# Kernel tuning notes

Measured on AMD Instinct MI355X. Metric: run time of the kernel, lower is better.

Reference implementation:

```python
import jax, jax.numpy as jnp
import numpy as np
import math

B = 2
H = 16
M = 1024
D = 64      # head_dim
P = 1024    # persistent memory size
SPAN = 1024 # external attention span


def setup_inputs() -> dict:
    key = jax.random.key(0)
    k1, k2, k3, k4 = jax.random.split(key, 4)
    query = jax.random.normal(k1, (B * H, M, D), dtype=jnp.float32)
    attn = jax.random.normal(k2, (B * H, M, SPAN), dtype=jnp.float32)
    # params as in __init__
    pkey = jax.random.normal(k3, (H, D, P), dtype=jnp.float32) / math.sqrt(D)
    pval = jax.random.normal(k4, (H, P, D), dtype=jnp.float32) / math.sqrt(P)
    return {"query": query, "attn": attn, "key": pkey, "val": pval}


def reference(query, attn, key, val):
    h, d, p = key.shape
    bh, m, _ = query.shape
    q = query.reshape(-1, h, m, d)                      # [B,H,M,D]
    # attn_pers = q @ (key * sqrt(d)); later divided by sqrt(d) -> net q@key
    attn_pers = jnp.einsum('bhmd,hdp->bhmp', q, key * math.sqrt(d))
    attn_pers = attn_pers.reshape(-1, m, p)             # [B*H,M,P]
    scores = jnp.concatenate([attn, attn_pers], axis=-1) / math.sqrt(d)
    probs = jax.nn.softmax(scores, axis=-1)             # [B*H,M,SPAN+P]
    attn_out = probs[:, :, :-p]                         # [B*H,M,SPAN]
    pers = probs[:, :, -p:].reshape(-1, h, m, p)        # [B,H,M,P]
    out = jnp.einsum('bhmp,hpd->bhmd', pers, val * math.sqrt(p))
    out = out.reshape(-1, m, d)                         # [B*H,M,D]
    return (attn_out, out)
```

## Files before the change

### kernel.cpp

```cpp
#include <hip/hip_runtime.h>
#include <hip/hip_bf16.h>
#include <math.h>

#define BH   32
#define NH   16
#define MM   1024
#define DD   64
#define PP   1024
#define SPAN 1024

typedef unsigned short ushort_t;
typedef __attribute__((ext_vector_type(8))) short  short8;
typedef __attribute__((ext_vector_type(4))) float  f32x4;

#define MFMA(a,b,c) __builtin_amdgcn_mfma_f32_16x16x32_bf16(a,b,c,0,0,0)

#if __has_builtin(__builtin_amdgcn_exp2f)
#define EXP2(x) __builtin_amdgcn_exp2f(x)
#else
#define EXP2(x) __expf((x) * 0.6931471805599453f)
#endif

#define ATTN_SC 0.18033688011111603f
#define LOG2E   1.4426950408889634f

#define WS_SA_OFF  (4194304ull)
#define WS_SP0_OFF (4325376ull)
#define WS_SP1_OFF (4456448ull)
#define WS_O1_OFF  (4587520ull)
#define WS_NEED    (12976128ull)

__device__ __forceinline__ ushort_t f2bf(float x) {
    __hip_bfloat16 b = __float2bfloat16(x);
    return __builtin_bit_cast(unsigned short, b);
}
__device__ __forceinline__ float bf2f(ushort_t u) {
    __hip_bfloat16 b = __builtin_bit_cast(__hip_bfloat16, u);
    return __bfloat162float(b);
}

__launch_bounds__(256)
__global__ void pm_pre(const float* __restrict__ key,
                       const float* __restrict__ val,
                       ushort_t* __restrict__ wsKV)
{
    int bi = blockIdx.x, t = threadIdx.x;
    if (bi < 512) {
        int id = bi * 256 + t;
        int l  = id & 63;
        int ks = (id >> 6) & 1;
        int pb = (id >> 7) & 3;
        int c  = (id >> 9) & 15;
        int h  = (id >> 13) & 15;
        int p     = c * 64 + pb * 16 + (l & 15);
        int dbase = ks * 32 + (l >> 4) * 8;
        size_t fo = (size_t)(h * 16 + c) * 8192 + (size_t)(pb * 2 + ks) * 512 + (size_t)l * 8;
#pragma unroll
        for (int e = 0; e < 8; ++e)
            wsKV[fo + e] = f2bf(key[(size_t)(h * 64 + dbase + e) * PP + p] * LOG2E);
    } else {
        int id = (bi - 512) * 256 + t;
        int l   = id & 63;
        int db  = (id >> 6) & 3;
        int ks2 = (id >> 8) & 1;
        int c   = (id >> 9) & 15;
        int h   = (id >> 13) & 15;
        int d = db * 16 + (l & 15);
        size_t fo = (size_t)(h * 16 + c) * 8192 + 4096 + (size_t)(ks2 * 4 + db) * 512 + (size_t)l * 8;
#pragma unroll
        for (int e = 0; e < 8; ++e) {
            int p = c * 64 + ks2 * 32 + ((l >> 4) * 4) + (e & 3) + 16 * (e >> 2);
            wsKV[fo + e] = f2bf(val[(size_t)(h * PP + p) * DD + d]);
        }
    }
}

__launch_bounds__(256)
__global__ void pm_work(const float* __restrict__ q,
                        const float* __restrict__ attn,
                        const ushort_t* __restrict__ wsKV,
                        float* __restrict__ ws_sa,
                        float* __restrict__ ws_sp0,
                        float* __restrict__ ws_sp1,
                        float* __restrict__ o1,
                        float* __restrict__ out)
{
    __shared__ ushort_t kvbuf[2][8192];

    const int t  = threadIdx.x;
    const int w  = t >> 6;
    const int l  = t & 63;
    const int bi = blockIdx.x;
    const int hi = l >> 4;
    const int lo = l & 15;

    const int ty   = bi % 3;
    const int unit = bi / 3;
    const int bh   = unit & 31;
    const int tile = unit >> 5;
    const size_t rowbase = (size_t)bh * MM + tile * 64;

    if (ty < 2) {
        const int s = ty;
        const int h = bh & (NH - 1);

        short8 qf[2][2];
        {
            const float* qr = q + (rowbase + w * 16 + lo) * DD + hi * 8;
#pragma unroll
            for (int ks = 0; ks < 2; ++ks) {
                float4 a = *(const float4*)(qr + ks * 32);
                float4 b = *(const float4*)(qr + ks * 32 + 4);
                float f[8] = {a.x, a.y, a.z, a.w, b.x, b.y, b.z, b.w};
                short8 qh, ql;
#pragma unroll
                for (int e = 0; e < 8; ++e) {
                    ushort_t hh = f2bf(f[e]);
                    qh[e] = (short)hh;
                    ql[e] = (short)f2bf(f[e] - bf2f(hh));
                }
                qf[ks][0] = qh;
                qf[ks][1] = ql;
            }
        }

        const ushort_t* KVb = wsKV + (size_t)h * (16 * 8192);

        auto STAGE = [&](int b, int c) {
            const char* src = (const char*)(KVb + (size_t)c * 8192) + w * 4096 + l * 16;
            char* dst = (char*)&kvbuf[b][0] + w * 4096;
#pragma unroll
            for (int j = 0; j < 4; ++j)
                __builtin_amdgcn_global_load_lds(
                    (const __attribute__((address_space(1))) void*)(src + j * 1024),
                    (__attribute__((address_space(3))) void*)(dst + j * 1024),
                    16, 0, 0);
        };

        f32x4 oacc[4] = {{0.f,0.f,0.f,0.f},{0.f,0.f,0.f,0.f},{0.f,0.f,0.f,0.f},{0.f,0.f,0.f,0.f}};
        float spart = 0.f;

        STAGE(0, s * 8);
        __syncthreads();

        for (int cc = 0; cc < 8; ++cc) {
            const int cur = cc & 1;
            if (cc < 7) STAGE(cur ^ 1, s * 8 + cc + 1);

            const ushort_t* Kc = &kvbuf[cur][0];
            const ushort_t* Vc = Kc + 4096;

            f32x4 sacc[4] = {{0.f,0.f,0.f,0.f},{0.f,0.f,0.f,0.f},{0.f,0.f,0.f,0.f},{0.f,0.f,0.f,0.f}};
            __builtin_amdgcn_s_setprio(1);
#pragma unroll
            for (int pb = 0; pb < 4; ++pb) {
#pragma unroll
                for (int ks = 0; ks < 2; ++ks) {
                    short8 khi = *(const short8*)(Kc + (pb * 2 + ks) * 512 + l * 8);
                    sacc[pb] = MFMA(khi, qf[ks][0], sacc[pb]);
                    sacc[pb] = MFMA(khi, qf[ks][1], sacc[pb]);
                }
            }
            __builtin_amdgcn_s_setprio(0);

            float ep[4][4];
#pragma unroll
            for (int pb = 0; pb < 4; ++pb)
#pragma unroll
                for (int r = 0; r < 4; ++r) {
                    float pv = EXP2(sacc[pb][r]);
                    ep[pb][r] = pv;
                    spart += pv;
                }

            short8 pf[2][2];
#pragma unroll
            for (int ks2 = 0; ks2 < 2; ++ks2) {
                short8 phi8, plo8;
#pragma unroll
                for (int e = 0; e < 8; ++e) {
                    float pv = ep[ks2 * 2 + (e >> 2)][e & 3];
                    ushort_t hh = f2bf(pv);
                    phi8[e] = (short)hh;
                    plo8[e] = (short)f2bf(pv - bf2f(hh));
                }
                pf[ks2][0] = phi8;
                pf[ks2][1] = plo8;
            }

            __builtin_amdgcn_s_setprio(1);
#pragma unroll
            for (int ks2 = 0; ks2 < 2; ++ks2) {
#pragma unroll
                for (int db = 0; db < 4; ++db) {
                    short8 vhi = *(const short8*)(Vc + (ks2 * 4 + db) * 512 + l * 8);
                    oacc[db] = MFMA(pf[ks2][0], vhi, oacc[db]);
                    oacc[db] = MFMA(pf[ks2][1], vhi, oacc[db]);
                }
            }
            __builtin_amdgcn_s_setprio(0);

            __syncthreads();
        }

        spart += __shfl_xor(spart, 16);
        spart += __shfl_xor(spart, 32);
        float* spdst = s ? ws_sp1 : ws_sp0;
        if (hi == 0) spdst[rowbase + w * 16 + lo] = spart;

        float* odst = s ? o1 : out;
#pragma unroll
        for (int reg = 0; reg < 4; ++reg) {
            const size_t ro = (rowbase + w * 16 + hi * 4 + reg) * DD + lo;
#pragma unroll
            for (int db = 0; db < 4; ++db)
                __builtin_nontemporal_store(oacc[db][reg], &odst[ro + db * 16]);
        }
    } else {
        for (int rp = 0; rp < 8; ++rp) {
            const int r0 = w * 16 + rp * 2;
            const f32x4* a0 = (const f32x4*)(attn + (rowbase + r0) * SPAN);
            const f32x4* a1 = (const f32x4*)(attn + (rowbase + r0 + 1) * SPAN);
            f32x4 v0[4], v1[4];
#pragma unroll
            for (int j = 0; j < 4; ++j) v0[j] = a0[j * 64 + l];
#pragma unroll
            for (int j = 0; j < 4; ++j) v1[j] = a1[j * 64 + l];

            float s0 = 0.f, s1 = 0.f;
#pragma unroll
            for (int j = 0; j < 4; ++j)
#pragma unroll
                for (int e = 0; e < 4; ++e) {
                    s0 += EXP2(v0[j][e] * ATTN_SC);
                    s1 += EXP2(v1[j][e] * ATTN_SC);
                }
#pragma unroll
            for (int s = 1; s < 64; s <<= 1) {
                s0 += __shfl_xor(s0, s);
                s1 += __shfl_xor(s1, s);
            }
            if (l == 0) {
                ws_sa[rowbase + r0]     = s0;
                ws_sa[rowbase + r0 + 1] = s1;
            }
        }
    }
}

__launch_bounds__(256)
__global__ void pm_norm(const float* __restrict__ attn,
                        const float* __restrict__ ws_sa,
                        const float* __restrict__ ws_sp0,
                        const float* __restrict__ ws_sp1,
                        const float* __restrict__ o1,
                        float* __restrict__ attn_out,
                        float* __restrict__ out)
{
    const int t = threadIdx.x;
    const int w = t >> 6;
    const int l = t & 63;
    const size_t row = (size_t)blockIdx.x * 4 + w;

    const float iZ = 1.f / (ws_sa[row] + ws_sp0[row] + ws_sp1[row]);

    const f32x4* arow = (const f32x4*)(attn + row * SPAN);
    f32x4 av[4];
#pragma unroll
    for (int j = 0; j < 4; ++j) av[j] = arow[j * 64 + l];
    const float ov0 = out[row * DD + l];
    const float ov1 = o1[row * DD + l];

    f32x4* orow = (f32x4*)(attn_out + row * SPAN);
#pragma unroll
    for (int j = 0; j < 4; ++j) {
        f32x4 o;
#pragma unroll
        for (int e = 0; e < 4; ++e) o[e] = EXP2(av[j][e] * ATTN_SC) * iZ;
        __builtin_nontemporal_store(o, orow + j * 64 + l);
    }
    __builtin_nontemporal_store((ov0 + ov1) * 32.f * iZ, &out[row * DD + l]);
}

__launch_bounds__(256)
__global__ void pm_fallback(const float* __restrict__ q,
                            const float* __restrict__ attn,
                            const float* __restrict__ key,
                            const float* __restrict__ val,
                            float* __restrict__ attn_out,
                            float* __restrict__ out)
{
    __shared__ float qs[64][68];
    __shared__ float ks[64][68];
    __shared__ float vs[64][DD];
    __shared__ float sc[64][66];
    __shared__ float rmax[64];
    __shared__ float rsum[64];

    const int t    = threadIdx.x;
    const int bh   = blockIdx.y;
    const int tile = blockIdx.x;
    const int h    = bh & (NH - 1);
    const int m0   = tile * 64;
    const int tr   = t >> 4;
    const int tc   = t & 15;
    const int r0   = tr * 4;
    const int c0   = tc * 4;
    const int lane = t & 63;
    const int wave = t >> 6;

    const size_t qbase = (size_t)bh * MM * DD + (size_t)m0 * DD;
    const size_t abase = (size_t)bh * MM * SPAN + (size_t)m0 * SPAN;
    const size_t kbase = (size_t)h * DD * PP;
    const size_t vbase = (size_t)h * PP * DD;

#pragma unroll
    for (int j = 0; j < 16; ++j) {
        int idx = j * 256 + t;
        int r = idx >> 6, d = idx & 63;
        qs[r][d] = q[qbase + (size_t)r * DD + d];
    }
    for (int rr = 0; rr < 16; ++rr) {
        int r = wave * 16 + rr;
        const float* arow = attn + abase + (size_t)r * SPAN;
        float av[16];
        float mx = -INFINITY;
#pragma unroll
        for (int j = 0; j < 16; ++j) { av[j] = arow[j * 64 + lane] * 0.125f; mx = fmaxf(mx, av[j]); }
#pragma unroll
        for (int s = 32; s; s >>= 1) mx = fmaxf(mx, __shfl_xor(mx, s));
        float sm = 0.f;
#pragma unroll
        for (int j = 0; j < 16; ++j) sm += __expf(av[j] - mx);
#pragma unroll
        for (int s = 32; s; s >>= 1) sm += __shfl_xor(sm, s);
        if (lane == 0) { rmax[r] = mx; rsum[r] = sm; }
    }
    __syncthreads();
    for (int p0 = 0; p0 < PP; p0 += 64) {
        if (p0) __syncthreads();
#pragma unroll
        for (int j = 0; j < 16; ++j) {
            int idx = j * 256 + t;
            int d = idx >> 6, pc = idx & 63;
            ks[pc][d] = key[kbase + (size_t)d * PP + p0 + pc];
        }
        __syncthreads();
        float acc[4][4] = {};
#pragma unroll
        for (int d0 = 0; d0 < DD; d0 += 4) {
            float4 q4[4], k4[4];
#pragma unroll
            for (int rr = 0; rr < 4; ++rr) q4[rr] = *(const float4*)&qs[r0 + rr][d0];
#pragma unroll
            for (int cc = 0; cc < 4; ++cc) k4[cc] = *(const float4*)&ks[c0 + cc][d0];
#pragma unroll
            for (int rr = 0; rr < 4; ++rr)
#pragma unroll
                for (int cc = 0; cc < 4; ++cc)
                    acc[rr][cc] += q4[rr].x * k4[cc].x + q4[rr].y * k4[cc].y
                                 + q4[rr].z * k4[cc].z + q4[rr].w * k4[cc].w;
        }
#pragma unroll
        for (int rr = 0; rr < 4; ++rr) {
            float mx = fmaxf(fmaxf(acc[rr][0], acc[rr][1]), fmaxf(acc[rr][2], acc[rr][3]));
#pragma unroll
            for (int s = 8; s; s >>= 1) mx = fmaxf(mx, __shfl_xor(mx, s));
            float sm = 0.f;
#pragma unroll
            for (int cc = 0; cc < 4; ++cc) sm += __expf(acc[rr][cc] - mx);
#pragma unroll
            for (int s = 8; s; s >>= 1) sm += __shfl_xor(sm, s);
            if (tc == 0) {
                int r = r0 + rr;
                float om = rmax[r], os = rsum[r];
                float nm = fmaxf(om, mx);
                rsum[r] = os * __expf(om - nm) + sm * __expf(mx - nm);
                rmax[r] = nm;
            }
        }
    }
    __syncthreads();
    for (int rr = 0; rr < 16; ++rr) {
        int r = wave * 16 + rr;
        float Mx = rmax[r];
        float iZ = 1.0f / rsum[r];
        const float* arow = attn + abase + (size_t)r * SPAN;
        float* orow = attn_out + abase + (size_t)r * SPAN;
#pragma unroll
        for (int j = 0; j < 16; ++j) {
            float a = arow[j * 64 + lane] * 0.125f;
            orow[j * 64 + lane] = __expf(a - Mx) * iZ;
        }
    }
    float acc2[4][4] = {};
    for (int p0 = 0; p0 < PP; p0 += 64) {
        __syncthreads();
#pragma unroll
        for (int j = 0; j < 16; ++j) {
            int idx = j * 256 + t;
            int d = idx >> 6, pc = idx & 63;
            ks[pc][d] = key[kbase + (size_t)d * PP + p0 + pc];
        }
#pragma unroll
        for (int j = 0; j < 16; ++j) {
            int idx = j * 256 + t;
            int pc = idx >> 6, d = idx & 63;
            vs[pc][d] = val[vbase + (size_t)(p0 + pc) * DD + d];
        }
        __syncthreads();
        float acc[4][4] = {};
#pragma unroll
        for (int d0 = 0; d0 < DD; d0 += 4) {
            float4 q4[4], k4[4];
#pragma unroll
            for (int rr = 0; rr < 4; ++rr) q4[rr] = *(const float4*)&qs[r0 + rr][d0];
#pragma unroll
            for (int cc = 0; cc < 4; ++cc) k4[cc] = *(const float4*)&ks[c0 + cc][d0];
#pragma unroll
            for (int rr = 0; rr < 4; ++rr)
#pragma unroll
                for (int cc = 0; cc < 4; ++cc)
                    acc[rr][cc] += q4[rr].x * k4[cc].x + q4[rr].y * k4[cc].y
                                 + q4[rr].z * k4[cc].z + q4[rr].w * k4[cc].w;
        }
#pragma unroll
        for (int rr = 0; rr < 4; ++rr) {
            float Mx = rmax[r0 + rr];
#pragma unroll
            for (int cc = 0; cc < 4; ++cc)
                sc[r0 + rr][c0 + cc] = __expf(acc[rr][cc] - Mx);
        }
        __syncthreads();
        for (int pc = 0; pc < 64; ++pc) {
            float4 v4 = *(const float4*)&vs[pc][tc * 4];
#pragma unroll
            for (int rr = 0; rr < 4; ++rr) {
                float pr = sc[r0 + rr][pc];
                acc2[rr][0] += pr * v4.x;
                acc2[rr][1] += pr * v4.y;
                acc2[rr][2] += pr * v4.z;
                acc2[rr][3] += pr * v4.w;
            }
        }
    }
#pragma unroll
    for (int rr = 0; rr < 4; ++rr) {
        int r = r0 + rr;
        float s = 32.0f / rsum[r];
        float4 o;
        o.x = acc2[rr][0] * s; o.y = acc2[rr][1] * s;
        o.z = acc2[rr][2] * s; o.w = acc2[rr][3] * s;
        *(float4*)&out[(size_t)bh * MM * DD + (size_t)(m0 + r) * DD + tc * 4] = o;
    }
}

extern "C" void kernel_launch(void* const* d_in, const int* in_sizes, int n_in,
                              void* d_out, int out_size, void* d_ws, size_t ws_size,
                              hipStream_t stream) {
    const float* q    = (const float*)d_in[0];
    const float* attn = (const float*)d_in[1];
    const float* key  = (const float*)d_in[2];
    const float* val  = (const float*)d_in[3];
    float* attn_out = (float*)d_out;
    float* out      = (float*)d_out + (size_t)BH * MM * SPAN;

    if (ws_size >= WS_NEED) {
        ushort_t* wsKV   = (ushort_t*)d_ws;
        float*    ws_sa  = (float*)((char*)d_ws + WS_SA_OFF);
        float*    ws_sp0 = (float*)((char*)d_ws + WS_SP0_OFF);
        float*    ws_sp1 = (float*)((char*)d_ws + WS_SP1_OFF);
        float*    o1     = (float*)((char*)d_ws + WS_O1_OFF);
        pm_pre <<<1024, 256, 0, stream>>>(key, val, wsKV);
        pm_work<<<1536, 256, 0, stream>>>(q, attn, wsKV, ws_sa, ws_sp0, ws_sp1, o1, out);
        pm_norm<<<8192, 256, 0, stream>>>(attn, ws_sa, ws_sp0, ws_sp1, o1, attn_out, out);
    } else {
        dim3 grid(MM / 64, BH);
        pm_fallback<<<grid, 256, 0, stream>>>(q, attn, key, val, attn_out, out);
    }
}
```

Before: 87.85 us.

## Fuse attn row-sum into normalization kernel to avoid re-reading attn

```diff
diff --git a/kernel.cpp b/kernel.cpp
--- a/kernel.cpp
+++ b/kernel.cpp
@@ -24,11 +24,10 @@
 #define ATTN_SC 0.18033688011111603f
 #define LOG2E   1.4426950408889634f
 
-#define WS_SA_OFF  (4194304ull)
-#define WS_SP0_OFF (4325376ull)
-#define WS_SP1_OFF (4456448ull)
-#define WS_O1_OFF  (4587520ull)
-#define WS_NEED    (12976128ull)
+#define WS_SP0_OFF (4194304ull)
+#define WS_SP1_OFF (4325376ull)
+#define WS_O1_OFF  (4456448ull)
+#define WS_NEED    (12845056ull)
 
 __device__ __forceinline__ ushort_t f2bf(float x) {
     __hip_bfloat16 b = __float2bfloat16(x);
@@ -76,14 +75,12 @@
 }
 
 __launch_bounds__(256)
-__global__ void pm_work(const float* __restrict__ q,
-                        const float* __restrict__ attn,
-                        const ushort_t* __restrict__ wsKV,
-                        float* __restrict__ ws_sa,
-                        float* __restrict__ ws_sp0,
-                        float* __restrict__ ws_sp1,
-                        float* __restrict__ o1,
-                        float* __restrict__ out)
+__global__ void pm_flash(const float* __restrict__ q,
+                         const ushort_t* __restrict__ wsKV,
+                         float* __restrict__ ws_sp0,
+                         float* __restrict__ ws_sp1,
+                         float* __restrict__ o1,
+                         float* __restrict__ out)
 {
     __shared__ ushort_t kvbuf[2][8192];
 
@@ -94,163 +91,129 @@
     const int hi = l >> 4;
     const int lo = l & 15;
 
-    const int ty   = bi % 3;
-    const int unit = bi / 3;
+    const int s    = bi & 1;
+    const int unit = bi >> 1;
     const int bh   = unit & 31;
     const int tile = unit >> 5;
+    const int h    = bh & (NH - 1);
     const size_t rowbase = (size_t)bh * MM + tile * 64;
 
-    if (ty < 2) {
-        const int s = ty;
-        const int h = bh & (NH - 1);
-
-        short8 qf[2][2];
-        {
-            const float* qr = q + (rowbase + w * 16 + lo) * DD + hi * 8;
+    short8 qf[2][2];
+    {
+        const float* qr = q + (rowbase + w * 16 + lo) * DD + hi * 8;
+#pragma unroll
+        for (int ks = 0; ks < 2; ++ks) {
+            float4 a = *(const float4*)(qr + ks * 32);
+            float4 b = *(const float4*)(qr + ks * 32 + 4);
+            float f[8] = {a.x, a.y, a.z, a.w, b.x, b.y, b.z, b.w};
+            short8 qh, ql;
+#pragma unroll
+            for (int e = 0; e < 8; ++e) {
+                ushort_t hh = f2bf(f[e]);
+                qh[e] = (short)hh;
+                ql[e] = (short)f2bf(f[e] - bf2f(hh));
+            }
+            qf[ks][0] = qh;
+            qf[ks][1] = ql;
+        }
+    }
+
+    const ushort_t* KVb = wsKV + (size_t)h * (16 * 8192);
+
+    auto STAGE = [&](int b, int c) {
+        const char* src = (const char*)(KVb + (size_t)c * 8192) + w * 4096 + l * 16;
+        char* dst = (char*)&kvbuf[b][0] + w * 4096;
+#pragma unroll
+        for (int j = 0; j < 4; ++j)
+            __builtin_amdgcn_global_load_lds(
+                (const __attribute__((address_space(1))) void*)(src + j * 1024),
+                (__attribute__((address_space(3))) void*)(dst + j * 1024),
+                16, 0, 0);
+    };
+
+    f32x4 oacc[4] = {{0.f,0.f,0.f,0.f},{0.f,0.f,0.f,0.f},{0.f,0.f,0.f,0.f},{0.f,0.f,0.f,0.f}};
+    float spart = 0.f;
+
+    STAGE(0, s * 8);
+    __syncthreads();
+
+    for (int cc = 0; cc < 8; ++cc) {
+        const int cur = cc & 1;
+        if (cc < 7) STAGE(cur ^ 1, s * 8 + cc + 1);
+
+        const ushort_t* Kc = &kvbuf[cur][0];
+        const ushort_t* Vc = Kc + 4096;
+
+        f32x4 sacc[4] = {{0.f,0.f,0.f,0.f},{0.f,0.f,0.f,0.f},{0.f,0.f,0.f,0.f},{0.f,0.f,0.f,0.f}};
+        __builtin_amdgcn_s_setprio(1);
+#pragma unroll
+        for (int pb = 0; pb < 4; ++pb) {
 #pragma unroll
             for (int ks = 0; ks < 2; ++ks) {
-                float4 a = *(const float4*)(qr + ks * 32);
-                float4 b = *(const float4*)(qr + ks * 32 + 4);
-                float f[8] = {a.x, a.y, a.z, a.w, b.x, b.y, b.z, b.w};
-                short8 qh, ql;
-#pragma unroll
-                for (int e = 0; e < 8; ++e) {
-                    ushort_t hh = f2bf(f[e]);
-                    qh[e] = (short)hh;
-                    ql[e] = (short)f2bf(f[e] - bf2f(hh));
-                }
-                qf[ks][0] = qh;
-                qf[ks][1] = ql;
-            }
-        }
-
-        const ushort_t* KVb = wsKV + (size_t)h * (16 * 8192);
-
-        auto STAGE = [&](int b, int c) {
-            const char* src = (const char*)(KVb + (size_t)c * 8192) + w * 4096 + l * 16;
-            char* dst = (char*)&kvbuf[b][0] + w * 4096;
-#pragma unroll
-            for (int j = 0; j < 4; ++j)
-                __builtin_amdgcn_global_load_lds(
-                    (const __attribute__((address_space(1))) void*)(src + j * 1024),
-                    (__attribute__((address_space(3))) void*)(dst + j * 1024),
-                    16, 0, 0);
-        };
-
-        f32x4 oacc[4] = {{0.f,0.f,0.f,0.f},{0.f,0.f,0.f,0.f},{0.f,0.f,0.f,0.f},{0.f,0.f,0.f,0.f}};
-        float spart = 0.f;
-
-        STAGE(0, s * 8);
+                short8 khi = *(const short8*)(Kc + (pb * 2 + ks) * 512 + l * 8);
+                sacc[pb] = MFMA(khi, qf[ks][0], sacc[pb]);
+                sacc[pb] = MFMA(khi, qf[ks][1], sacc[pb]);
+            }
+        }
+        __builtin_amdgcn_s_setprio(0);
+
+        float ep[4][4];
+#pragma unroll
+        for (int pb = 0; pb < 4; ++pb)
+#pragma unroll
+            for (int r = 0; r < 4; ++r) {
+                float pv = EXP2(sacc[pb][r]);
+                ep[pb][r] = pv;
+                spart += pv;
+            }
+
+        short8 pf[2][2];
+#pragma unroll
+        for (int ks2 = 0; ks2 < 2; ++ks2) {
+            short8 phi8, plo8;
+#pragma unroll
+            for (int e = 0; e < 8; ++e) {
+                float pv = ep[ks2 * 2 + (e >> 2)][e & 3];
+                ushort_t hh = f2bf(pv);
+                phi8[e] = (short)hh;
+                plo8[e] = (short)f2bf(pv - bf2f(hh));
+            }
+            pf[ks2][0] = phi8;
+            pf[ks2][1] = plo8;
+        }
+
+        __builtin_amdgcn_s_setprio(1);
+#pragma unroll
+        for (int ks2 = 0; ks2 < 2; ++ks2) {
+#pragma unroll
+            for (int db = 0; db < 4; ++db) {
+                short8 vhi = *(const short8*)(Vc + (ks2 * 4 + db) * 512 + l * 8);
+                oacc[db] = MFMA(pf[ks2][0], vhi, oacc[db]);
+                oacc[db] = MFMA(pf[ks2][1], vhi, oacc[db]);
+            }
+        }
+        __builtin_amdgcn_s_setprio(0);
+
         __syncthreads();
-
-        for (int cc = 0; cc < 8; ++cc) {
-            const int cur = cc & 1;
-            if (cc < 7) STAGE(cur ^ 1, s * 8 + cc + 1);
-
-            const ushort_t* Kc = &kvbuf[cur][0];
-            const ushort_t* Vc = Kc + 4096;
-
-            f32x4 sacc[4] = {{0.f,0.f,0.f,0.f},{0.f,0.f,0.f,0.f},{0.f,0.f,0.f,0.f},{0.f,0.f,0.f,0.f}};
-            __builtin_amdgcn_s_setprio(1);
-#pragma unroll
-            for (int pb = 0; pb < 4; ++pb) {
-#pragma unroll
-                for (int ks = 0; ks < 2; ++ks) {
-                    short8 khi = *(const short8*)(Kc + (pb * 2 + ks) * 512 + l * 8);
-                    sacc[pb] = MFMA(khi, qf[ks][0], sacc[pb]);
-                    sacc[pb] = MFMA(khi, qf[ks][1], sacc[pb]);
-                }
-            }
-            __builtin_amdgcn_s_setprio(0);
-
-            float ep[4][4];
-#pragma unroll
-            for (int pb = 0; pb < 4; ++pb)
-#pragma unroll
-                for (int r = 0; r < 4; ++r) {
-                    float pv = EXP2(sacc[pb][r]);
-                    ep[pb][r] = pv;
-                    spart += pv;
-                }
-
-            short8 pf[2][2];
-#pragma unroll
-            for (int ks2 = 0; ks2 < 2; ++ks2) {
-                short8 phi8, plo8;
-#pragma unroll
-                for (int e = 0; e < 8; ++e) {
-                    float pv = ep[ks2 * 2 + (e >> 2)][e & 3];
-                    ushort_t hh = f2bf(pv);
-                    phi8[e] = (short)hh;
-                    plo8[e] = (short)f2bf(pv - bf2f(hh));
-                }
-                pf[ks2][0] = phi8;
-                pf[ks2][1] = plo8;
-            }
-
-            __builtin_amdgcn_s_setprio(1);
-#pragma unroll
-            for (int ks2 = 0; ks2 < 2; ++ks2) {
-#pragma unroll
-                for (int db = 0; db < 4; ++db) {
-                    short8 vhi = *(const short8*)(Vc + (ks2 * 4 + db) * 512 + l * 8);
-                    oacc[db] = MFMA(pf[ks2][0], vhi, oacc[db]);
-                    oacc[db] = MFMA(pf[ks2][1], vhi, oacc[db]);
-                }
-            }
-            __builtin_amdgcn_s_setprio(0);
-
-            __syncthreads();
-        }
-
-        spart += __shfl_xor(spart, 16);
-        spart += __shfl_xor(spart, 32);
-        float* spdst = s ? ws_sp1 : ws_sp0;
-        if (hi == 0) spdst[rowbase + w * 16 + lo] = spart;
-
-        float* odst = s ? o1 : out;
-#pragma unroll
-        for (int reg = 0; reg < 4; ++reg) {
-            const size_t ro = (rowbase + w * 16 + hi * 4 + reg) * DD + lo;
-#pragma unroll
-            for (int db = 0; db < 4; ++db)
-                __builtin_nontemporal_store(oacc[db][reg], &odst[ro + db * 16]);
-        }
-    } else {
-        for (int rp = 0; rp < 8; ++rp) {
-            const int r0 = w * 16 + rp * 2;
-            const f32x4* a0 = (const f32x4*)(attn + (rowbase + r0) * SPAN);
-            const f32x4* a1 = (const f32x4*)(attn + (rowbase + r0 + 1) * SPAN);
-            f32x4 v0[4], v1[4];
-#pragma unroll
-            for (int j = 0; j < 4; ++j) v0[j] = a0[j * 64 + l];
-#pragma unroll
-            for (int j = 0; j < 4; ++j) v1[j] = a1[j * 64 + l];
-
-            float s0 = 0.f, s1 = 0.f;
-#pragma unroll
-            for (int j = 0; j < 4; ++j)
-#pragma unroll
-                for (int e = 0; e < 4; ++e) {
-                    s0 += EXP2(v0[j][e] * ATTN_SC);
-                    s1 += EXP2(v1[j][e] * ATTN_SC);
-                }
-#pragma unroll
-            for (int s = 1; s < 64; s <<= 1) {
-                s0 += __shfl_xor(s0, s);
-                s1 += __shfl_xor(s1, s);
-            }
-            if (l == 0) {
-                ws_sa[rowbase + r0]     = s0;
-                ws_sa[rowbase + r0 + 1] = s1;
-            }
-        }
+    }
+
+    spart += __shfl_xor(spart, 16);
+    spart += __shfl_xor(spart, 32);
+    float* spdst = s ? ws_sp1 : ws_sp0;
+    if (hi == 0) spdst[rowbase + w * 16 + lo] = spart;
+
+    float* odst = s ? o1 : out;
+#pragma unroll
+    for (int reg = 0; reg < 4; ++reg) {
+        const size_t ro = (rowbase + w * 16 + hi * 4 + reg) * DD + lo;
+#pragma unroll
+        for (int db = 0; db < 4; ++db)
+            __builtin_nontemporal_store(oacc[db][reg], &odst[ro + db * 16]);
     }
 }
 
 __launch_bounds__(256)
 __global__ void pm_norm(const float* __restrict__ attn,
-                        const float* __restrict__ ws_sa,
                         const float* __restrict__ ws_sp0,
                         const float* __restrict__ ws_sp1,
                         const float* __restrict__ o1,
@@ -262,23 +225,31 @@
     const int l = t & 63;
     const size_t row = (size_t)blockIdx.x * 4 + w;
 
-    const float iZ = 1.f / (ws_sa[row] + ws_sp0[row] + ws_sp1[row]);
-
     const f32x4* arow = (const f32x4*)(attn + row * SPAN);
     f32x4 av[4];
 #pragma unroll
     for (int j = 0; j < 4; ++j) av[j] = arow[j * 64 + l];
+
+    float sm = 0.f;
+#pragma unroll
+    for (int j = 0; j < 4; ++j)
+#pragma unroll
+        for (int e = 0; e < 4; ++e) {
+            av[j][e] = EXP2(av[j][e] * ATTN_SC);
+            sm += av[j][e];
+        }
+#pragma unroll
+    for (int s = 1; s < 64; s <<= 1) sm += __shfl_xor(sm, s);
+
+    const float iZ = 1.f / (sm + ws_sp0[row] + ws_sp1[row]);
+
+    f32x4* orow = (f32x4*)(attn_out + row * SPAN);
+#pragma unroll
+    for (int j = 0; j < 4; ++j)
+        __builtin_nontemporal_store(av[j] * iZ, orow + j * 64 + l);
+
     const float ov0 = out[row * DD + l];
     const float ov1 = o1[row * DD + l];
-
-    f32x4* orow = (f32x4*)(attn_out + row * SPAN);
-#pragma unroll
-    for (int j = 0; j < 4; ++j) {
-        f32x4 o;
-#pragma unroll
-        for (int e = 0; e < 4; ++e) o[e] = EXP2(av[j][e] * ATTN_SC) * iZ;
-        __builtin_nontemporal_store(o, orow + j * 64 + l);
-    }
     __builtin_nontemporal_store((ov0 + ov1) * 32.f * iZ, &out[row * DD + l]);
 }
 
@@ -384,13 +355,13 @@
     for (int rr = 0; rr < 16; ++rr) {
         int r = wave * 16 + rr;
         float Mx = rmax[r];
-        float iZ = 1.0f / rsum[r];
+        float iZv = 1.0f / rsum[r];
         const float* arow = attn + abase + (size_t)r * SPAN;
         float* orow = attn_out + abase + (size_t)r * SPAN;
 #pragma unroll
         for (int j = 0; j < 16; ++j) {
             float a = arow[j * 64 + lane] * 0.125f;
-            orow[j * 64 + lane] = __expf(a - Mx) * iZ;
+            orow[j * 64 + lane] = __expf(a - Mx) * iZv;
         }
     }
     float acc2[4][4] = {};
@@ -467,13 +438,12 @@
 
     if (ws_size >= WS_NEED) {
         ushort_t* wsKV   = (ushort_t*)d_ws;
-        float*    ws_sa  = (float*)((char*)d_ws + WS_SA_OFF);
         float*    ws_sp0 = (float*)((char*)d_ws + WS_SP0_OFF);
         float*    ws_sp1 = (float*)((char*)d_ws + WS_SP1_OFF);
         float*    o1     = (float*)((char*)d_ws + WS_O1_OFF);
-        pm_pre <<<1024, 256, 0, stream>>>(key, val, wsKV);
-        pm_work<<<1536, 256, 0, stream>>>(q, attn, wsKV, ws_sa, ws_sp0, ws_sp1, o1, out);
-        pm_norm<<<8192, 256, 0, stream>>>(attn, ws_sa, ws_sp0, ws_sp1, o1, attn_out, out);
+        pm_pre  <<<1024, 256, 0, stream>>>(key, val, wsKV);
+        pm_flash<<<1024, 256, 0, stream>>>(q, wsKV, ws_sp0, ws_sp1, o1, out);
+        pm_norm <<<8192, 256, 0, stream>>>(attn, ws_sp0, ws_sp1, o1, attn_out, out);
     } else {
         dim3 grid(MM / 64, BH);
         pm_fallback<<<grid, 256, 0, stream>>>(q, attn, key, val, attn_out, out);
```

Result: faster. 75.54 us (median of 2 runs) (-14.0%).
